# Performance work log

Measured on AMD Instinct MI355X. Metric: run time of the kernel, lower is better.

Reference implementation:

```python
import jax, jax.numpy as jnp
import numpy as np

B, S = 8, 2048
CHANNELS, DIM, HEADS = 256, 3, 6
TCH = CHANNELS * 2  # 512
EPS = 1e-5


def _linear_init(key, out_f, in_f):
    # torch nn.Linear default init: U(-1/sqrt(in_f), 1/sqrt(in_f)) for W and b
    k1, k2 = jax.random.split(key)
    bound = 1.0 / np.sqrt(in_f)
    w = jax.random.uniform(k1, (out_f, in_f), jnp.float32, -bound, bound)
    b = jax.random.uniform(k2, (out_f,), jnp.float32, -bound, bound)
    return w, b


def setup_inputs() -> dict:
    key = jax.random.key(0)
    ks = jax.random.split(key, 8)
    x = jax.random.normal(ks[0], (B, S, TCH), jnp.float32)
    wq, bq = _linear_init(ks[1], DIM, TCH)
    wk, bk = _linear_init(ks[2], DIM, TCH)
    wv, bv = _linear_init(ks[3], DIM, TCH)
    wo, bo = _linear_init(ks[4], TCH, HEADS * DIM)
    w1, b1 = _linear_init(ks[5], TCH, TCH)
    w2, b2 = _linear_init(ks[6], TCH, TCH)
    gamma = jnp.ones((TCH,), jnp.float32)
    beta = jnp.zeros((TCH,), jnp.float32)
    return {"x": x, "wq": wq, "bq": bq, "wk": wk, "bk": bk, "wv": wv, "bv": bv,
            "wo": wo, "bo": bo, "w1": w1, "b1": b1, "w2": w2, "b2": b2,
            "gamma": gamma, "beta": beta}


def _layernorm(x, gamma, beta):
    mu = jnp.mean(x, axis=-1, keepdims=True)
    var = jnp.mean(jnp.square(x - mu), axis=-1, keepdims=True)
    return (x - mu) * jax.lax.rsqrt(var + EPS) * gamma + beta


def reference(x, wq, bq, wk, bk, wv, bv, wo, bo, w1, b1, w2, b2, gamma, beta):
    # All heads share the same w_q/w_k/w_v, so one attention pass suffices;
    # concatenating HEADS copies reproduces the original math exactly.
    q = x @ wq.T + bq                      # [B,S,DIM]
    k = x @ wk.T + bk                      # [B,S,DIM]
    v = x @ wv.T + bv                      # [B,S,DIM]
    scores = jnp.einsum('bqd,bkd->bqk', q, k) / np.sqrt(DIM)  # [B,S,S]
    soft = jax.nn.softmax(scores, axis=-1)
    z = jnp.einsum('bqk,bkd->bqd', soft, v)  # [B,S,DIM]
    z = jnp.concatenate([z] * HEADS, axis=-1)  # [B,S,HEADS*DIM]
    z = z @ wo.T + bo                       # [B,S,TCH]
    r0 = x + (z @ w1.T + b1)
    r1 = _layernorm(r0, gamma, beta)
    r1 = r1 @ w2.T + b2
    r = r0 + r1
    return _layernorm(r, gamma, beta)
```

## Files before the change

### kernel.cpp

```cpp
#include <hip/hip_runtime.h>
#include <hip/hip_bf16.h>

#define TCH 512
#define MTOT 16384
#define SEQ 2048
#define LN_EPS 1e-5f

typedef __attribute__((ext_vector_type(8))) __bf16 bf16x8;
typedef __attribute__((ext_vector_type(4))) float f32x4;

__device__ __forceinline__ unsigned pkbf(float a, float b) {
  union { __hip_bfloat16 h; unsigned short u; } ca, cb;
  ca.h = __float2bfloat16(a); cb.h = __float2bfloat16(b);
  return (unsigned)ca.u | ((unsigned)cb.u << 16);
}
__device__ __forceinline__ float bf_lo(unsigned u) { return __uint_as_float(u << 16); }
__device__ __forceinline__ float bf_hi(unsigned u) { return __uint_as_float(u & 0xffff0000u); }

__device__ __forceinline__ bf16x8 cvt8(float4 a, float4 b) {
  union { __hip_bfloat16 h; __bf16 v; } u;
  bf16x8 r;
  u.h = __float2bfloat16(a.x); r[0] = u.v;
  u.h = __float2bfloat16(a.y); r[1] = u.v;
  u.h = __float2bfloat16(a.z); r[2] = u.v;
  u.h = __float2bfloat16(a.w); r[3] = u.v;
  u.h = __float2bfloat16(b.x); r[4] = u.v;
  u.h = __float2bfloat16(b.y); r[5] = u.v;
  u.h = __float2bfloat16(b.z); r[6] = u.v;
  u.h = __float2bfloat16(b.w); r[7] = u.v;
  return r;
}

#define QSCALE 0.8329517853860118f

__global__ __launch_bounds__(256) void prep_kernel(
    const float* __restrict__ w2,
    const float* __restrict__ wo, const float* __restrict__ bo,
    const float* __restrict__ wq, const float* __restrict__ bq,
    const float* __restrict__ wk, const float* __restrict__ bk,
    const float* __restrict__ wv, const float* __restrict__ bv,
    __hip_bfloat16* __restrict__ w2b,
    float4* __restrict__ wo_eff4,
    __hip_bfloat16* __restrict__ wqkvb, float* __restrict__ qkvbias)
{
  int i = blockIdx.x * 256 + threadIdx.x;
  w2b[i] = __float2bfloat16(w2[i]);
  if (i < TCH) {
    float s0 = 0.f, s1 = 0.f, s2 = 0.f;
    #pragma unroll
    for (int h = 0; h < 6; ++h) {
      s0 += wo[i*18 + h*3 + 0];
      s1 += wo[i*18 + h*3 + 1];
      s2 += wo[i*18 + h*3 + 2];
    }
    wo_eff4[i] = make_float4(s0, s1, s2, bo[i]);
  }
  if (i < 16 * TCH) {
    int row = i >> 9, k = i & 511;
    float v;
    if      (row < 3) v = wq[row * TCH + k] * QSCALE;
    else if (row < 6) v = wk[(row - 3) * TCH + k];
    else if (row < 9) v = wv[(row - 6) * TCH + k];
    else              v = 0.f;
    wqkvb[i] = __float2bfloat16(v);
  }
  if (i < 16) {
    float v;
    if      (i < 3) v = bq[i] * QSCALE;
    else if (i < 6) v = bk[i - 3];
    else if (i < 9) v = bv[i - 6];
    else            v = 0.f;
    qkvbias[i] = v;
  }
}

__global__ __launch_bounds__(256) void prep2_kernel(
    const float* __restrict__ w1, const float* __restrict__ b1,
    const float4* __restrict__ wo_eff4, float4* __restrict__ weff4)
{
  const int t = threadIdx.x, w = t >> 6, l = t & 63;
  const int i = blockIdx.x * 4 + w;
  float sx = 0.f, sy = 0.f, sz = 0.f, sw = 0.f;
  #pragma unroll
  for (int j = 0; j < 8; ++j) {
    const int k = j * 64 + l;
    const float a = w1[(size_t)i * TCH + k];
    const float4 e = wo_eff4[k];
    sx += a * e.x; sy += a * e.y; sz += a * e.z; sw += a * e.w;
  }
  #pragma unroll
  for (int off = 1; off < 64; off <<= 1) {
    sx += __shfl_xor(sx, off, 64);
    sy += __shfl_xor(sy, off, 64);
    sz += __shfl_xor(sz, off, 64);
    sw += __shfl_xor(sw, off, 64);
  }
  if (l == 0) weff4[i] = make_float4(sx, sy, sz, sw + b1[i]);
}

__global__ __launch_bounds__(256) void qkv_kernel(
    const float* __restrict__ x,
    const __hip_bfloat16* __restrict__ wqkvb, const float* __restrict__ qkvbias,
    float4* __restrict__ q4, uint4* __restrict__ kvp)
{
  const int t = threadIdx.x, wv = t >> 6, ln = t & 63;
  const int l16 = ln & 15, quad = ln >> 4;
  const int row0 = blockIdx.x * 16;
  const int k0 = wv * 128;

  bf16x8 bfr[4];
  #pragma unroll
  for (int ks = 0; ks < 4; ++ks)
    bfr[ks] = *reinterpret_cast<const bf16x8*>(wqkvb + l16 * TCH + k0 + ks * 32 + quad * 8);

  const float* xp = x + (size_t)(row0 + l16) * TCH + k0 + quad * 8;

  f32x4 acc = {};
  #pragma unroll
  for (int ks = 0; ks < 4; ++ks) {
    float4 a = *(const float4*)(xp + ks * 32);
    float4 b = *(const float4*)(xp + ks * 32 + 4);
    acc = __builtin_amdgcn_mfma_f32_16x16x32_bf16(cvt8(a, b), bfr[ks], acc, 0, 0, 0);
  }

  __shared__ float tr[4][16][17];
  __shared__ float fin[16][17];
  #pragma unroll
  for (int r = 0; r < 4; ++r) tr[wv][quad * 4 + r][l16] = acc[r];
  __syncthreads();

  {
    const int r = t >> 4, c = t & 15;
    fin[r][c] = tr[0][r][c] + tr[1][r][c] + tr[2][r][c] + tr[3][r][c] + qkvbias[c];
  }
  __syncthreads();

  if (t < 16) {
    q4[row0 + t] = make_float4(fin[t][0], fin[t][1], fin[t][2], 0.f);
  } else if (t < 32) {
    const int r = t - 16;
    kvp[row0 + r] = make_uint4(pkbf(fin[r][3], fin[r][4]),
                               pkbf(fin[r][5], fin[r][6]),
                               pkbf(fin[r][7], fin[r][8]), 0u);
  }
}

__global__ __launch_bounds__(1024) void attn_kernel(
    const float4* __restrict__ q4, const uint4* __restrict__ kvp,
    const float* __restrict__ x, const float4* __restrict__ weff4,
    const float* __restrict__ gamma, const float* __restrict__ beta,
    __hip_bfloat16* __restrict__ r0b, __hip_bfloat16* __restrict__ r1b)
{
  __shared__ float4 part[16 * 64];
  __shared__ float4 zbuf[64];

  const int b    = blockIdx.x >> 5;
  const int qc   = blockIdx.x & 31;
  const int base = b * SEQ;
  const int tid  = threadIdx.x;
  const int wave = tid >> 6;
  const int lane = tid & 63;
  const float4 q = q4[base + qc * 64 + lane];

  const int wu = __builtin_amdgcn_readfirstlane(wave);
  const uint4* kvw = kvp + base + wu * 128;

  float l[4] = {}, a0[4] = {}, a1[4] = {}, a2[4] = {};
  #pragma unroll 4
  for (int i = 0; i < 32; ++i) {
    #pragma unroll
    for (int s = 0; s < 4; ++s) {
      uint4 rec = kvw[s * 32 + i];
      float sc = bf_lo(rec.x) * q.x + bf_hi(rec.x) * q.y + bf_lo(rec.y) * q.z;
      float p = __builtin_amdgcn_exp2f(sc);
      l[s]  += p;
      a0[s] += p * bf_hi(rec.y);
      a1[s] += p * bf_lo(rec.z);
      a2[s] += p * bf_hi(rec.z);
    }
  }
  part[wave * 64 + lane] = make_float4(l[0]+l[1]+l[2]+l[3],
                                       a0[0]+a0[1]+a0[2]+a0[3],
                                       a1[0]+a1[1]+a1[2]+a1[3],
                                       a2[0]+a2[1]+a2[2]+a2[3]);
  __syncthreads();

  if (tid < 64) {
    float L = 0.f, A0 = 0.f, A1 = 0.f, A2 = 0.f;
    #pragma unroll
    for (int w = 0; w < 16; ++w) {
      float4 p = part[w * 64 + tid];
      L += p.x; A0 += p.y; A1 += p.z; A2 += p.w;
    }
    const float inv = 1.f / L;
    zbuf[tid] = make_float4(A0 * inv, A1 * inv, A2 * inv, 0.f);
  }
  __syncthreads();

  const int c0 = lane * 8;
  float4 wv[8];
  #pragma unroll
  for (int j = 0; j < 8; ++j) wv[j] = weff4[c0 + j];
  const float4 g0  = *(const float4*)(gamma + c0);
  const float4 g1  = *(const float4*)(gamma + c0 + 4);
  const float4 be0 = *(const float4*)(beta  + c0);
  const float4 be1 = *(const float4*)(beta  + c0 + 4);
  const float gg[8] = {g0.x,g0.y,g0.z,g0.w,g1.x,g1.y,g1.z,g1.w};
  const float bb[8] = {be0.x,be0.y,be0.z,be0.w,be1.x,be1.y,be1.z,be1.w};

  #pragma unroll
  for (int qi = 0; qi < 4; ++qi) {
    const int qloc = wave * 4 + qi;
    const int grow = base + qc * 64 + qloc;
    const float4 z = zbuf[qloc];
    const float* xr = x + (size_t)grow * TCH + c0;
    const float4 x0 = *(const float4*)xr;
    const float4 x1 = *(const float4*)(xr + 4);
    const float xv[8] = {x0.x,x0.y,x0.z,x0.w,x1.x,x1.y,x1.z,x1.w};
    float r0v[8], s = 0.f, sq = 0.f;
    #pragma unroll
    for (int j = 0; j < 8; ++j) {
      float v = xv[j] + z.x * wv[j].x + z.y * wv[j].y + z.z * wv[j].z + wv[j].w;
      r0v[j] = v; s += v; sq += v * v;
    }
    #pragma unroll
    for (int off = 1; off < 64; off <<= 1) {
      s  += __shfl_xor(s,  off, 64);
      sq += __shfl_xor(sq, off, 64);
    }
    const float mu = s * (1.f / TCH);
    const float rs = rsqrtf(sq * (1.f / TCH) - mu * mu + LN_EPS);
    *(bf16x8*)(r0b + (size_t)grow * TCH + c0) =
        cvt8(make_float4(r0v[0], r0v[1], r0v[2], r0v[3]),
             make_float4(r0v[4], r0v[5], r0v[6], r0v[7]));
    float r1v[8];
    #pragma unroll
    for (int j = 0; j < 8; ++j) r1v[j] = (r0v[j] - mu) * rs * gg[j] + bb[j];
    *(bf16x8*)(r1b + (size_t)grow * TCH + c0) =
        cvt8(make_float4(r1v[0], r1v[1], r1v[2], r1v[3]),
             make_float4(r1v[4], r1v[5], r1v[6], r1v[7]));
  }
}

__global__ __launch_bounds__(512) void gemm2_kernel(
    const __hip_bfloat16* __restrict__ A,
    const __hip_bfloat16* __restrict__ W,
    const float* __restrict__ bias,
    const __hip_bfloat16* __restrict__ res,
    const float* __restrict__ gamma, const float* __restrict__ beta,
    float* __restrict__ out)
{
  __shared__ float redS[32][4], redQ[32][4];
  __shared__ float muL[32], rsL[32];

  const int row0 = blockIdx.x * 32;
  const int t    = threadIdx.x;
  const int w    = t >> 6;
  const int l    = t & 63;
  const int l16  = l & 15, quad = l >> 4;
  const int wr   = w >> 2, wc = w & 3;

  const __hip_bfloat16* Ap = A + (size_t)(row0 + wr * 16 + l16) * TCH + quad * 8;
  const __hip_bfloat16* Wp = W + (size_t)(wc * 128 + l16) * TCH + quad * 8;

  f32x4 acc[8] = {};
  #pragma unroll
  for (int ks = 0; ks < 16; ++ks) {
    bf16x8 af = *reinterpret_cast<const bf16x8*>(Ap + ks * 32);
    #pragma unroll
    for (int n = 0; n < 8; ++n) {
      bf16x8 bfv = *reinterpret_cast<const bf16x8*>(Wp + (size_t)n * 16 * TCH + ks * 32);
      acc[n] = __builtin_amdgcn_mfma_f32_16x16x32_bf16(af, bfv, acc[n], 0, 0, 0);
    }
  }

  #pragma unroll
  for (int r = 0; r < 4; ++r) {
    const int lrow = wr * 16 + quad * 4 + r;
    const int grow = row0 + lrow;
    float s = 0.f, sq = 0.f;
    #pragma unroll
    for (int n = 0; n < 8; ++n) {
      const int col = wc * 128 + n * 16 + l16;
      float v = acc[n][r] + bias[col] +
                __bfloat162float(res[(size_t)grow * TCH + col]);
      acc[n][r] = v; s += v; sq += v * v;
    }
    #pragma unroll
    for (int off = 1; off < 16; off <<= 1) {
      s  += __shfl_xor(s,  off, 64);
      sq += __shfl_xor(sq, off, 64);
    }
    if (l16 == 0) { redS[lrow][wc] = s; redQ[lrow][wc] = sq; }
  }
  __syncthreads();
  if (t < 32) {
    const float S = redS[t][0] + redS[t][1] + redS[t][2] + redS[t][3];
    const float Q = redQ[t][0] + redQ[t][1] + redQ[t][2] + redQ[t][3];
    const float mu = S * (1.f / TCH);
    muL[t] = mu;
    rsL[t] = rsqrtf(Q * (1.f / TCH) - mu * mu + LN_EPS);
  }
  __syncthreads();
  #pragma unroll
  for (int r = 0; r < 4; ++r) {
    const int lrow = wr * 16 + quad * 4 + r;
    const int grow = row0 + lrow;
    const float mu = muL[lrow], rs = rsL[lrow];
    #pragma unroll
    for (int n = 0; n < 8; ++n) {
      const int col = wc * 128 + n * 16 + l16;
      out[(size_t)grow * TCH + col] =
          (acc[n][r] - mu) * rs * gamma[col] + beta[col];
    }
  }
}

extern "C" void kernel_launch(void* const* d_in, const int* in_sizes, int n_in,
                              void* d_out, int out_size, void* d_ws, size_t ws_size,
                              hipStream_t stream) {
  (void)in_sizes; (void)n_in; (void)out_size; (void)ws_size;
  const float* x     = (const float*)d_in[0];
  const float* wq    = (const float*)d_in[1];
  const float* bq    = (const float*)d_in[2];
  const float* wk    = (const float*)d_in[3];
  const float* bk    = (const float*)d_in[4];
  const float* wv    = (const float*)d_in[5];
  const float* bv    = (const float*)d_in[6];
  const float* wo    = (const float*)d_in[7];
  const float* bo    = (const float*)d_in[8];
  const float* w1    = (const float*)d_in[9];
  const float* b1    = (const float*)d_in[10];
  const float* w2    = (const float*)d_in[11];
  const float* b2    = (const float*)d_in[12];
  const float* gamma = (const float*)d_in[13];
  const float* beta  = (const float*)d_in[14];
  float* out = (float*)d_out;

  char* ws = (char*)d_ws;
  size_t off = 0;
  float4* q4      = (float4*)(ws + off); off += (size_t)MTOT * 16;
  uint4*  kvp     = (uint4*)(ws + off);  off += (size_t)MTOT * 16;
  float4* wo_eff4 = (float4*)(ws + off); off += (size_t)TCH * 16;
  float4* weff4   = (float4*)(ws + off); off += (size_t)TCH * 16;
  __hip_bfloat16* w2b   = (__hip_bfloat16*)(ws + off); off += (size_t)TCH * TCH * 2;
  __hip_bfloat16* wqkvb = (__hip_bfloat16*)(ws + off); off += (size_t)16 * TCH * 2;
  float*          qkvbias = (float*)(ws + off);        off += 64;
  __hip_bfloat16* r0b = (__hip_bfloat16*)(ws + off); off += (size_t)MTOT * TCH * 2;
  __hip_bfloat16* r1b = (__hip_bfloat16*)(ws + off); off += (size_t)MTOT * TCH * 2;

  prep_kernel<<<(TCH*TCH)/256, 256, 0, stream>>>(
      w2, wo, bo, wq, bq, wk, bk, wv, bv, w2b, wo_eff4, wqkvb, qkvbias);
  prep2_kernel<<<TCH/4, 256, 0, stream>>>(w1, b1, wo_eff4, weff4);
  qkv_kernel<<<MTOT/16, 256, 0, stream>>>(x, wqkvb, qkvbias, q4, kvp);
  attn_kernel<<<MTOT/64, 1024, 0, stream>>>(q4, kvp, x, weff4, gamma, beta, r0b, r1b);
  gemm2_kernel<<<MTOT/32, 512, 0, stream>>>(r1b, w2b, b2, r0b, gamma, beta, out);
}
```

Before: 209.5 us.

## Tile final GEMM 128x128 with LDS double-buffering and split LayerNorm into separate kernel

Result: faster. 178.1 us (-15.0%).

```diff
diff --git a/kernel.cpp b/kernel.cpp
--- a/kernel.cpp
+++ b/kernel.cpp
@@ -242,77 +242,135 @@
   }
 }
 
-__global__ __launch_bounds__(512) void gemm2_kernel(
+__global__ __launch_bounds__(256) void gemm_kernel(
     const __hip_bfloat16* __restrict__ A,
     const __hip_bfloat16* __restrict__ W,
     const float* __restrict__ bias,
     const __hip_bfloat16* __restrict__ res,
+    __hip_bfloat16* __restrict__ Cout,
+    float2* __restrict__ partial)
+{
+  __shared__ __align__(16) __hip_bfloat16 At[2][4][128][8];
+  __shared__ __align__(16) __hip_bfloat16 Wt[2][4][128][8];
+  __shared__ float redS[128][2];
+  __shared__ float redQ[128][2];
+
+  const int bx   = blockIdx.x;
+  const int rb   = bx & 127, cb = bx >> 7;
+  const int row0 = rb * 128, col0 = cb * 128;
+  const int t    = threadIdx.x;
+  const int w    = t >> 6, l = t & 63;
+  const int l16  = l & 15, quad = l >> 4;
+  const int wr   = w >> 1, wc = w & 1;
+  const int srow = t & 127;
+  const int sq0  = (t >> 7) << 1;
+
+  auto stage = [&](int ks, int b) {
+    #pragma unroll
+    for (int j = 0; j < 2; ++j) {
+      const int q = sq0 | j;
+      __builtin_amdgcn_global_load_lds(
+          (const __attribute__((address_space(1))) void*)(A + (size_t)(row0 + srow) * TCH + ks * 32 + q * 8),
+          (__attribute__((address_space(3))) void*)&At[b][q][srow][0], 16, 0, 0);
+      __builtin_amdgcn_global_load_lds(
+          (const __attribute__((address_space(1))) void*)(W + (size_t)(col0 + srow) * TCH + ks * 32 + q * 8),
+          (__attribute__((address_space(3))) void*)&Wt[b][q][srow][0], 16, 0, 0);
+    }
+  };
+
+  f32x4 acc[4][4] = {};
+  stage(0, 0);
+  for (int ks = 0; ks < 16; ++ks) {
+    const int cur = ks & 1;
+    __syncthreads();
+    if (ks < 15) stage(ks + 1, cur ^ 1);
+    bf16x8 af[4], bf[4];
+    #pragma unroll
+    for (int mt = 0; mt < 4; ++mt)
+      af[mt] = *reinterpret_cast<const bf16x8*>(&At[cur][quad][wr * 64 + mt * 16 + l16][0]);
+    #pragma unroll
+    for (int nt = 0; nt < 4; ++nt)
+      bf[nt] = *reinterpret_cast<const bf16x8*>(&Wt[cur][quad][wc * 64 + nt * 16 + l16][0]);
+    #pragma unroll
+    for (int mt = 0; mt < 4; ++mt)
+      #pragma unroll
+      for (int nt = 0; nt < 4; ++nt)
+        acc[mt][nt] = __builtin_amdgcn_mfma_f32_16x16x32_bf16(af[mt], bf[nt], acc[mt][nt], 0, 0, 0);
+  }
+
+  #pragma unroll
+  for (int mt = 0; mt < 4; ++mt) {
+    #pragma unroll
+    for (int r = 0; r < 4; ++r) {
+      const int lrow = wr * 64 + mt * 16 + quad * 4 + r;
+      const int grow = row0 + lrow;
+      float s = 0.f, sq = 0.f;
+      #pragma unroll
+      for (int nt = 0; nt < 4; ++nt) {
+        const int col = col0 + wc * 64 + nt * 16 + l16;
+        float v = acc[mt][nt][r] + bias[col] + __bfloat162float(res[(size_t)grow * TCH + col]);
+        Cout[(size_t)grow * TCH + col] = __float2bfloat16(v);
+        s += v; sq += v * v;
+      }
+      #pragma unroll
+      for (int off = 1; off < 16; off <<= 1) {
+        s  += __shfl_xor(s,  off, 64);
+        sq += __shfl_xor(sq, off, 64);
+      }
+      if (l16 == 0) { redS[lrow][wc] = s; redQ[lrow][wc] = sq; }
+    }
+  }
+  __syncthreads();
+
+  if (t < 128) {
+    partial[(size_t)cb * MTOT + row0 + t] =
+        make_float2(redS[t][0] + redS[t][1], redQ[t][0] + redQ[t][1]);
+  }
+}
+
+template<typename OUT_T>
+__global__ __launch_bounds__(256) void ln_kernel(
+    const __hip_bfloat16* __restrict__ Cin, const float2* __restrict__ partial,
     const float* __restrict__ gamma, const float* __restrict__ beta,
-    float* __restrict__ out)
-{
-  __shared__ float redS[32][4], redQ[32][4];
-  __shared__ float muL[32], rsL[32];
-
-  const int row0 = blockIdx.x * 32;
-  const int t    = threadIdx.x;
-  const int w    = t >> 6;
-  const int l    = t & 63;
-  const int l16  = l & 15, quad = l >> 4;
-  const int wr   = w >> 2, wc = w & 3;
-
-  const __hip_bfloat16* Ap = A + (size_t)(row0 + wr * 16 + l16) * TCH + quad * 8;
-  const __hip_bfloat16* Wp = W + (size_t)(wc * 128 + l16) * TCH + quad * 8;
-
-  f32x4 acc[8] = {};
-  #pragma unroll
-  for (int ks = 0; ks < 16; ++ks) {
-    bf16x8 af = *reinterpret_cast<const bf16x8*>(Ap + ks * 32);
-    #pragma unroll
-    for (int n = 0; n < 8; ++n) {
-      bf16x8 bfv = *reinterpret_cast<const bf16x8*>(Wp + (size_t)n * 16 * TCH + ks * 32);
-      acc[n] = __builtin_amdgcn_mfma_f32_16x16x32_bf16(af, bfv, acc[n], 0, 0, 0);
-    }
-  }
-
-  #pragma unroll
-  for (int r = 0; r < 4; ++r) {
-    const int lrow = wr * 16 + quad * 4 + r;
-    const int grow = row0 + lrow;
-    float s = 0.f, sq = 0.f;
-    #pragma unroll
-    for (int n = 0; n < 8; ++n) {
-      const int col = wc * 128 + n * 16 + l16;
-      float v = acc[n][r] + bias[col] +
-                __bfloat162float(res[(size_t)grow * TCH + col]);
-      acc[n][r] = v; s += v; sq += v * v;
-    }
-    #pragma unroll
-    for (int off = 1; off < 16; off <<= 1) {
-      s  += __shfl_xor(s,  off, 64);
-      sq += __shfl_xor(sq, off, 64);
-    }
-    if (l16 == 0) { redS[lrow][wc] = s; redQ[lrow][wc] = sq; }
-  }
-  __syncthreads();
-  if (t < 32) {
-    const float S = redS[t][0] + redS[t][1] + redS[t][2] + redS[t][3];
-    const float Q = redQ[t][0] + redQ[t][1] + redQ[t][2] + redQ[t][3];
-    const float mu = S * (1.f / TCH);
-    muL[t] = mu;
-    rsL[t] = rsqrtf(Q * (1.f / TCH) - mu * mu + LN_EPS);
-  }
-  __syncthreads();
-  #pragma unroll
-  for (int r = 0; r < 4; ++r) {
-    const int lrow = wr * 16 + quad * 4 + r;
-    const int grow = row0 + lrow;
-    const float mu = muL[lrow], rs = rsL[lrow];
-    #pragma unroll
-    for (int n = 0; n < 8; ++n) {
-      const int col = wc * 128 + n * 16 + l16;
-      out[(size_t)grow * TCH + col] =
-          (acc[n][r] - mu) * rs * gamma[col] + beta[col];
-    }
+    OUT_T* __restrict__ out)
+{
+  const int t = threadIdx.x, wv = t >> 6, ln = t & 63;
+  const int row = blockIdx.x * 4 + wv;
+
+  float2 p0 = partial[row];
+  float2 p1 = partial[MTOT + row];
+  float2 p2 = partial[2 * MTOT + row];
+  float2 p3 = partial[3 * MTOT + row];
+  const float S = p0.x + p1.x + p2.x + p3.x;
+  const float Q = p0.y + p1.y + p2.y + p3.y;
+  const float mu  = S * (1.f / TCH);
+  const float var = Q * (1.f / TCH) - mu * mu;
+  const float rs  = rsqrtf(var + LN_EPS);
+
+  const int c0 = ln * 8;
+  bf16x8 vr = *reinterpret_cast<const bf16x8*>(Cin + (size_t)row * TCH + c0);
+  float4 g0 = *(const float4*)(gamma + c0), g1 = *(const float4*)(gamma + c0 + 4);
+  float4 b0 = *(const float4*)(beta  + c0), b1 = *(const float4*)(beta  + c0 + 4);
+
+  float o[8];
+  const float gg[8] = {g0.x,g0.y,g0.z,g0.w,g1.x,g1.y,g1.z,g1.w};
+  const float bb[8] = {b0.x,b0.y,b0.z,b0.w,b1.x,b1.y,b1.z,b1.w};
+  #pragma unroll
+  for (int j = 0; j < 8; ++j) {
+    union { __bf16 v; __hip_bfloat16 h; } u; u.v = vr[j];
+    o[j] = (__bfloat162float(u.h) - mu) * rs * gg[j] + bb[j];
+  }
+
+  if constexpr (sizeof(OUT_T) == 2) {
+    unsigned ov[4];
+    #pragma unroll
+    for (int j = 0; j < 4; ++j) ov[j] = pkbf(o[2*j], o[2*j+1]);
+    *(uint4*)((__hip_bfloat16*)out + (size_t)row * TCH + c0) =
+        make_uint4(ov[0], ov[1], ov[2], ov[3]);
+  } else {
+    float* op = (float*)out + (size_t)row * TCH + c0;
+    *(float4*)op       = make_float4(o[0], o[1], o[2], o[3]);
+    *(float4*)(op + 4) = make_float4(o[4], o[5], o[6], o[7]);
   }
 }
 
@@ -348,11 +406,14 @@
   float*          qkvbias = (float*)(ws + off);        off += 64;
   __hip_bfloat16* r0b = (__hip_bfloat16*)(ws + off); off += (size_t)MTOT * TCH * 2;
   __hip_bfloat16* r1b = (__hip_bfloat16*)(ws + off); off += (size_t)MTOT * TCH * 2;
+  __hip_bfloat16* rrb = (__hip_bfloat16*)(ws + off); off += (size_t)MTOT * TCH * 2;
+  float2* part2 = (float2*)(ws + off); off += (size_t)4 * MTOT * 8;
 
   prep_kernel<<<(TCH*TCH)/256, 256, 0, stream>>>(
       w2, wo, bo, wq, bq, wk, bk, wv, bv, w2b, wo_eff4, wqkvb, qkvbias);
   prep2_kernel<<<TCH/4, 256, 0, stream>>>(w1, b1, wo_eff4, weff4);
   qkv_kernel<<<MTOT/16, 256, 0, stream>>>(x, wqkvb, qkvbias, q4, kvp);
   attn_kernel<<<MTOT/64, 1024, 0, stream>>>(q4, kvp, x, weff4, gamma, beta, r0b, r1b);
-  gemm2_kernel<<<MTOT/32, 512, 0, stream>>>(r1b, w2b, b2, r0b, gamma, beta, out);
-}
+  gemm_kernel<<<512, 256, 0, stream>>>(r1b, w2b, b2, r0b, rrb, part2);
+  ln_kernel<float><<<MTOT/4, 256, 0, stream>>>(rrb, part2, gamma, beta, out);
+}
```
